# Performance work log

Measured on AMD Instinct MI355X. Metric: run time of the kernel, lower is better.

## Reference

```python
import jax, jax.numpy as jnp
import numpy as np

B, C, H, W = 8, 10, 128, 128  # batch, hidden_dim, spatial
EPS = 1e-5


def conv1x1(x, w, b=None):
    # x: [b, i, h, w], w: [o, i] -> [b, o, h, w]
    y = jnp.einsum('oi,bihw->bohw', w, x)
    if b is not None:
        y = y + b[None, :, None, None]
    return y


def bn(x, gamma, beta):
    # training-mode batchnorm over (N, H, W), as InPlaceABNSync(activation='none')
    m = x.mean(axis=(0, 2, 3), keepdims=True)
    v = x.var(axis=(0, 2, 3), keepdims=True)
    xn = (x - m) * jax.lax.rsqrt(v + EPS)
    return xn * gamma[None, :, None, None] + beta[None, :, None, None]


def conv_gru(x, h, wg, bg, wc):
    # ConvGRU with 1x1 kernels: gates conv -> 2 channels (reset, update)
    gates = conv1x1(jnp.concatenate([x, h], axis=1), wg, bg)  # [b,2,h,w]
    reset = jax.nn.sigmoid(gates[:, 0:1])
    update = jax.nn.sigmoid(gates[:, 1:2])
    cand = jnp.tanh(conv1x1(jnp.concatenate([x, reset * h], axis=1), wc))
    return (1.0 - update) * h + update * cand


def setup_inputs() -> dict:
    key = jax.random.key(0)
    ks = jax.random.split(key, 16)
    rn = lambda k, shape, s=1.0: jax.random.normal(k, shape, dtype=jnp.float32) * s
    inp = {
        'f0': rn(ks[0], (B, C, H, W)),
        'f1': rn(ks[1], (B, C, H, W)),
        'h0': rn(ks[2], (B, C, H, W)),
        'h1': rn(ks[3], (B, C, H, W)),
        'h2': rn(ks[4], (B, C, H, W)),
        # Composition.comp_att: Conv2d(2C -> 1, bias=True) + Sigmoid
        'W_att': rn(ks[5], (1, 2 * C), 0.1),
        'b_att': jnp.zeros((1,), jnp.float32),
        # Composition.relation: Conv(2C->2C, no bias) BN ReLU Conv(2C->C, no bias) BN ReLU
        'W_r1': rn(ks[6], (2 * C, 2 * C), 0.1),
        'g_r1': jnp.ones((2 * C,), jnp.float32),
        'be_r1': jnp.zeros((2 * C,), jnp.float32),
        'W_r2': rn(ks[7], (C, 2 * C), 0.1),
        'g_r2': jnp.ones((C,), jnp.float32),
        'be_r2': jnp.zeros((C,), jnp.float32),
        # ConvGRU update[0]: gates Conv(2C->2, bias) ; candidate Conv(2C->C, no bias)
        'Wg0': rn(ks[8], (2, 2 * C), 0.1),
        'bg0': jnp.zeros((2,), jnp.float32),
        'Wc0': rn(ks[9], (C, 2 * C), 0.1),
        # ConvGRU update[1]
        'Wg1': rn(ks[10], (2, 2 * C), 0.1),
        'bg1': jnp.zeros((2,), jnp.float32),
        'Wc1': rn(ks[11], (C, 2 * C), 0.1),
    }
    return inp


def reference(f0, f1, h0, h1, h2,
              W_att, b_att, W_r1, g_r1, be_r1, W_r2, g_r2, be_r2,
              Wg0, bg0, Wc0, Wg1, bg1, Wc1):
    # node 0: update[0](h_node_list[0], f_node_list[0])
    node0 = conv_gru(h0, f0, Wg0, bg0, Wc0)
    # Composition over children h1, h2
    comp_att = jax.nn.sigmoid(conv1x1(jnp.concatenate([h1, h2], axis=1), W_att, b_att))  # [b,1,h,w]
    x = jnp.concatenate([f1, (h1 + h2) * comp_att], axis=1)  # [b,2C,h,w]
    x = jax.nn.relu(bn(conv1x1(x, W_r1), g_r1, be_r1))
    comp_full = jax.nn.relu(bn(conv1x1(x, W_r2), g_r2, be_r2))  # [b,C,h,w]
    # node 1: update[1](comp_full, f_node_list[1])
    node1 = conv_gru(comp_full, f1, Wg1, bg1, Wc1)
    return node0, node1, comp_att
```

## Files before the change

kernel.cpp:

```cpp
#include <hip/hip_runtime.h>
#include <math.h>

#define HW     16384
#define CDIM   10
#define NPIX   131072
#define NPLANE 1310720
#define BN_N   131072.0f
#define EPS_BN 1e-5f

__device__ __forceinline__ float sigf(float x) { return 1.0f / (1.0f + __expf(-x)); }
__device__ __forceinline__ float tanh_fast(float x) {
    x = fminf(fmaxf(x, -15.0f), 15.0f);
    float e = __expf(2.0f * x);
    return (e - 1.0f) / (e + 1.0f);
}
__device__ __forceinline__ float wred(float v) {
#pragma unroll
    for (int o = 32; o; o >>= 1) v += __shfl_down(v, o, 64);
    return v;
}

__global__ __launch_bounds__(256) void kernA(
    const float* __restrict__ f0, const float* __restrict__ f1,
    const float* __restrict__ h0, const float* __restrict__ h1, const float* __restrict__ h2,
    const float* __restrict__ W_att, const float* __restrict__ b_att,
    const float* __restrict__ W_r1,
    const float* __restrict__ Wg0, const float* __restrict__ bg0, const float* __restrict__ Wc0,
    float* __restrict__ node0, float* __restrict__ att_out, float* __restrict__ stats1)
{
    __shared__ float sW1[400], sWatt[20], sWg[40], sWc[200];
    __shared__ float sPart[4 * 40];
    const int tid = threadIdx.x;
    for (int i = tid; i < 400; i += 256) sW1[i] = W_r1[i];
    for (int i = tid; i < 200; i += 256) sWc[i] = Wc0[i];
    if (tid < 20) sWatt[tid] = W_att[tid];
    if (tid < 40) sWg[tid] = Wg0[tid];
    __syncthreads();
    const float batt = b_att[0], bg_r = bg0[0], bg_u = bg0[1];
    const int p = blockIdx.x * 256 + tid;
    const int b = p >> 14, s = p & 16383;
    const int base = b * (CDIM * HW) + s;
    const int wave = tid >> 6, lane = tid & 63;

    float vh1[10], vh2[10], vf1[10];
#pragma unroll
    for (int c = 0; c < 10; c++) {
        vh1[c] = h1[base + c * HW];
        vh2[c] = h2[base + c * HW];
        vf1[c] = f1[base + c * HW];
    }
    float z = batt;
#pragma unroll
    for (int c = 0; c < 10; c++) z += sWatt[c] * vh1[c] + sWatt[10 + c] * vh2[c];
    const float att = sigf(z);
    att_out[p] = att;

    float x[20];
#pragma unroll
    for (int c = 0; c < 10; c++) { x[c] = vf1[c]; x[10 + c] = (vh1[c] + vh2[c]) * att; }
#pragma unroll
    for (int o = 0; o < 20; o++) {
        float acc = 0.0f;
#pragma unroll
        for (int i = 0; i < 20; i++) acc = fmaf(sW1[o * 20 + i], x[i], acc);
        float q = acc * acc;
        float rs = wred(acc);
        float rq = wred(q);
        if (lane == 0) { sPart[wave * 40 + o] = rs; sPart[wave * 40 + 20 + o] = rq; }
    }
    __syncthreads();
    if (tid < 40) {
        float t = sPart[tid] + sPart[40 + tid] + sPart[80 + tid] + sPart[120 + tid];
        atomicAdd(&stats1[tid], t);
    }

    float vf0[10], vh0[10];
#pragma unroll
    for (int c = 0; c < 10; c++) { vf0[c] = f0[base + c * HW]; vh0[c] = h0[base + c * HW]; }
    float g0 = bg_r, g1 = bg_u;
#pragma unroll
    for (int i = 0; i < 10; i++) {
        g0 += sWg[i] * vh0[i] + sWg[10 + i] * vf0[i];
        g1 += sWg[20 + i] * vh0[i] + sWg[30 + i] * vf0[i];
    }
    const float r = sigf(g0), u = sigf(g1);
#pragma unroll
    for (int o = 0; o < 10; o++) {
        float acc = 0.0f;
#pragma unroll
        for (int i = 0; i < 10; i++) acc = fmaf(sWc[o * 20 + i], vh0[i], acc);
#pragma unroll
        for (int i = 0; i < 10; i++) acc = fmaf(sWc[o * 20 + 10 + i], r * vf0[i], acc);
        node0[base + o * HW] = (1.0f - u) * vf0[o] + u * tanh_fast(acc);
    }
}

__global__ __launch_bounds__(256) void kernC(
    const float* __restrict__ f1, const float* __restrict__ h1, const float* __restrict__ h2,
    const float* __restrict__ att_in,
    const float* __restrict__ W_r1, const float* __restrict__ g_r1, const float* __restrict__ be_r1,
    const float* __restrict__ W_r2,
    const float* __restrict__ stats1, float* __restrict__ y2out, float* __restrict__ stats2)
{
    __shared__ float sW1[400], sW2[200], sA[20], sB[20];
    __shared__ float sPart[4 * 20];
    const int tid = threadIdx.x;
    for (int i = tid; i < 400; i += 256) sW1[i] = W_r1[i];
    for (int i = tid; i < 200; i += 256) sW2[i] = W_r2[i];
    if (tid < 20) {
        float sm = stats1[tid], sq = stats1[20 + tid];
        float mean = sm * (1.0f / BN_N);
        float var = sq * (1.0f / BN_N) - mean * mean;
        float a = g_r1[tid] * rsqrtf(var + EPS_BN);
        sA[tid] = a;
        sB[tid] = be_r1[tid] - mean * a;
    }
    __syncthreads();
    const int p = blockIdx.x * 256 + tid;
    const int b = p >> 14, s = p & 16383;
    const int base = b * (CDIM * HW) + s;
    const int wave = tid >> 6, lane = tid & 63;

    float vh1[10], vh2[10], vf1[10];
#pragma unroll
    for (int c = 0; c < 10; c++) {
        vh1[c] = h1[base + c * HW];
        vh2[c] = h2[base + c * HW];
        vf1[c] = f1[base + c * HW];
    }
    const float att = att_in[p];
    float x[20];
#pragma unroll
    for (int c = 0; c < 10; c++) { x[c] = vf1[c]; x[10 + c] = (vh1[c] + vh2[c]) * att; }
    float x2[20];
#pragma unroll
    for (int o = 0; o < 20; o++) {
        float acc = 0.0f;
#pragma unroll
        for (int i = 0; i < 20; i++) acc = fmaf(sW1[o * 20 + i], x[i], acc);
        x2[o] = fmaxf(fmaf(sA[o], acc, sB[o]), 0.0f);
    }
    const int base2 = b * (10 * HW) + s;
#pragma unroll
    for (int o = 0; o < 10; o++) {
        float acc = 0.0f;
#pragma unroll
        for (int i = 0; i < 20; i++) acc = fmaf(sW2[o * 20 + i], x2[i], acc);
        y2out[base2 + o * HW] = acc;
        float q = acc * acc;
        float rs = wred(acc);
        float rq = wred(q);
        if (lane == 0) { sPart[wave * 20 + o] = rs; sPart[wave * 20 + 10 + o] = rq; }
    }
    __syncthreads();
    if (tid < 20) {
        float t = sPart[tid] + sPart[20 + tid] + sPart[40 + tid] + sPart[60 + tid];
        atomicAdd(&stats2[tid], t);
    }
}

__global__ __launch_bounds__(256) void kernE(
    const float* __restrict__ f1, const float* __restrict__ y2in,
    const float* __restrict__ stats2,
    const float* __restrict__ g_r2, const float* __restrict__ be_r2,
    const float* __restrict__ Wg1, const float* __restrict__ bg1, const float* __restrict__ Wc1,
    float* __restrict__ node1)
{
    __shared__ float sWg[40], sWc[200], sA[10], sB[10];
    const int tid = threadIdx.x;
    for (int i = tid; i < 200; i += 256) sWc[i] = Wc1[i];
    if (tid < 40) sWg[tid] = Wg1[tid];
    if (tid < 10) {
        float sm = stats2[tid], sq = stats2[10 + tid];
        float mean = sm * (1.0f / BN_N);
        float var = sq * (1.0f / BN_N) - mean * mean;
        float a = g_r2[tid] * rsqrtf(var + EPS_BN);
        sA[tid] = a;
        sB[tid] = be_r2[tid] - mean * a;
    }
    __syncthreads();
    const float bg_r = bg1[0], bg_u = bg1[1];
    const int p = blockIdx.x * 256 + tid;
    const int b = p >> 14, s = p & 16383;
    const int base = b * (CDIM * HW) + s;

    float comp[10], vf1[10];
#pragma unroll
    for (int c = 0; c < 10; c++) {
        vf1[c] = f1[base + c * HW];
        comp[c] = fmaxf(fmaf(sA[c], y2in[base + c * HW], sB[c]), 0.0f);
    }
    float g0 = bg_r, g1 = bg_u;
#pragma unroll
    for (int i = 0; i < 10; i++) {
        g0 += sWg[i] * comp[i] + sWg[10 + i] * vf1[i];
        g1 += sWg[20 + i] * comp[i] + sWg[30 + i] * vf1[i];
    }
    const float r = sigf(g0), u = sigf(g1);
#pragma unroll
    for (int o = 0; o < 10; o++) {
        float acc = 0.0f;
#pragma unroll
        for (int i = 0; i < 10; i++) acc = fmaf(sWc[o * 20 + i], comp[i], acc);
#pragma unroll
        for (int i = 0; i < 10; i++) acc = fmaf(sWc[o * 20 + 10 + i], r * vf1[i], acc);
        node1[base + o * HW] = (1.0f - u) * vf1[o] + u * tanh_fast(acc);
    }
}

extern "C" void kernel_launch(void* const* d_in, const int* in_sizes, int n_in,
                              void* d_out, int out_size, void* d_ws, size_t ws_size,
                              hipStream_t stream) {
    const float* f0    = (const float*)d_in[0];
    const float* f1    = (const float*)d_in[1];
    const float* h0    = (const float*)d_in[2];
    const float* h1    = (const float*)d_in[3];
    const float* h2    = (const float*)d_in[4];
    const float* W_att = (const float*)d_in[5];
    const float* b_att = (const float*)d_in[6];
    const float* W_r1  = (const float*)d_in[7];
    const float* g_r1  = (const float*)d_in[8];
    const float* be_r1 = (const float*)d_in[9];
    const float* W_r2  = (const float*)d_in[10];
    const float* g_r2  = (const float*)d_in[11];
    const float* be_r2 = (const float*)d_in[12];
    const float* Wg0   = (const float*)d_in[13];
    const float* bg0   = (const float*)d_in[14];
    const float* Wc0   = (const float*)d_in[15];
    const float* Wg1   = (const float*)d_in[16];
    const float* bg1   = (const float*)d_in[17];
    const float* Wc1   = (const float*)d_in[18];

    float* out   = (float*)d_out;
    float* node0 = out;
    float* node1 = out + NPLANE;
    float* attO  = out + 2 * NPLANE;

    float* y2     = (float*)d_ws;
    float* stats1 = y2 + (size_t)10 * NPIX;
    float* stats2 = stats1 + 40;

    hipMemsetAsync(stats1, 0, 64 * sizeof(float), stream);

    dim3 grid(NPIX / 256), blk(256);
    kernA<<<grid, blk, 0, stream>>>(f0, f1, h0, h1, h2, W_att, b_att, W_r1,
                                    Wg0, bg0, Wc0, node0, attO, stats1);
    kernC<<<grid, blk, 0, stream>>>(f1, h1, h2, attO, W_r1, g_r1, be_r1, W_r2,
                                    stats1, y2, stats2);
    kernE<<<grid, blk, 0, stream>>>(f1, y2, stats2, g_r2, be_r2, Wg1, bg1, Wc1,
                                    node1);
}
```

Baseline: 148.2 us.

## Fuse three kernels into one cooperative kernel with grid syncs for batchnorm stats

Replaces the three-kernel pipeline with a single cooperative kernel that computes each pixel's activations once and holds them in registers. Grid-wide syncs wait for each batchnorm's statistics to finish accumulating before the next stage uses them. This removes the re-reads of h1/h2/f1/att, the y2 workspace round trip and two kernel launches, roughly halving memory traffic. In exchange it relies on all 512 blocks being co-resident, pays the cost of two grid barriers, and caps occupancy at two blocks per CU, which could cause register pressure or spills.

```diff
diff --git a/kernel.cpp b/kernel.cpp
--- a/kernel.cpp
+++ b/kernel.cpp
@@ -1,5 +1,8 @@
 #include <hip/hip_runtime.h>
+#include <hip/hip_cooperative_groups.h>
 #include <math.h>
+
+namespace cg = cooperative_groups;
 
 #define HW     16384
 #define CDIM   10
@@ -19,234 +22,206 @@
     for (int o = 32; o; o >>= 1) v += __shfl_down(v, o, 64);
     return v;
 }
-
-__global__ __launch_bounds__(256) void kernA(
-    const float* __restrict__ f0, const float* __restrict__ f1,
-    const float* __restrict__ h0, const float* __restrict__ h1, const float* __restrict__ h2,
-    const float* __restrict__ W_att, const float* __restrict__ b_att,
-    const float* __restrict__ W_r1,
-    const float* __restrict__ Wg0, const float* __restrict__ bg0, const float* __restrict__ Wc0,
-    float* __restrict__ node0, float* __restrict__ att_out, float* __restrict__ stats1)
+__device__ __forceinline__ float agent_load(const float* a) {
+    return __hip_atomic_load(a, __ATOMIC_RELAXED, __HIP_MEMORY_SCOPE_AGENT);
+}
+
+struct P {
+    const float *f0, *f1, *h0, *h1, *h2;
+    const float *W_att, *b_att;
+    const float *W_r1, *g_r1, *be_r1, *W_r2, *g_r2, *be_r2;
+    const float *Wg0, *bg0, *Wc0, *Wg1, *bg1, *Wc1;
+    float *node0, *node1, *attO;
+    float *stats;
+};
+
+__global__ __launch_bounds__(256, 2) void fused(P p)
 {
-    __shared__ float sW1[400], sWatt[20], sWg[40], sWc[200];
-    __shared__ float sPart[4 * 40];
-    const int tid = threadIdx.x;
-    for (int i = tid; i < 400; i += 256) sW1[i] = W_r1[i];
-    for (int i = tid; i < 200; i += 256) sWc[i] = Wc0[i];
-    if (tid < 20) sWatt[tid] = W_att[tid];
-    if (tid < 40) sWg[tid] = Wg0[tid];
-    __syncthreads();
-    const float batt = b_att[0], bg_r = bg0[0], bg_u = bg0[1];
-    const int p = blockIdx.x * 256 + tid;
-    const int b = p >> 14, s = p & 16383;
+    cg::grid_group grid = cg::this_grid();
+    __shared__ float sW1[400], sW2[200], sWc0[200], sWc1[200];
+    __shared__ float sWatt[20], sWg0[40], sWg1[40];
+    __shared__ float sAB[80];
+    __shared__ float sPart[160];
+    const int tid  = threadIdx.x;
+    const int wave = tid >> 6, lane = tid & 63;
+
+    for (int i = tid; i < 400; i += 256) sW1[i] = p.W_r1[i];
+    for (int i = tid; i < 200; i += 256) {
+        sW2[i]  = p.W_r2[i];
+        sWc0[i] = p.Wc0[i];
+        sWc1[i] = p.Wc1[i];
+    }
+    if (tid < 20) sWatt[tid] = p.W_att[tid];
+    if (tid < 40) { sWg0[tid] = p.Wg0[tid]; sWg1[tid] = p.Wg1[tid]; }
+    __syncthreads();
+
+    const int px   = blockIdx.x * 256 + tid;
+    const int b    = px >> 14, s = px & 16383;
     const int base = b * (CDIM * HW) + s;
-    const int wave = tid >> 6, lane = tid & 63;
-
-    float vh1[10], vh2[10], vf1[10];
-#pragma unroll
-    for (int c = 0; c < 10; c++) {
-        vh1[c] = h1[base + c * HW];
-        vh2[c] = h2[base + c * HW];
-        vf1[c] = f1[base + c * HW];
-    }
-    float z = batt;
-#pragma unroll
-    for (int c = 0; c < 10; c++) z += sWatt[c] * vh1[c] + sWatt[10 + c] * vh2[c];
-    const float att = sigf(z);
-    att_out[p] = att;
 
     float x[20];
-#pragma unroll
-    for (int c = 0; c < 10; c++) { x[c] = vf1[c]; x[10 + c] = (vh1[c] + vh2[c]) * att; }
-#pragma unroll
-    for (int o = 0; o < 20; o++) {
-        float acc = 0.0f;
-#pragma unroll
-        for (int i = 0; i < 20; i++) acc = fmaf(sW1[o * 20 + i], x[i], acc);
-        float q = acc * acc;
-        float rs = wred(acc);
-        float rq = wred(q);
-        if (lane == 0) { sPart[wave * 40 + o] = rs; sPart[wave * 40 + 20 + o] = rq; }
+    {
+        float vh1[10], vh2[10];
+#pragma unroll
+        for (int c = 0; c < 10; c++) {
+            vh1[c]  = p.h1[base + c * HW];
+            vh2[c]  = p.h2[base + c * HW];
+            x[c]    = p.f1[base + c * HW];
+        }
+        float z = p.b_att[0];
+#pragma unroll
+        for (int c = 0; c < 10; c++) z += sWatt[c] * vh1[c] + sWatt[10 + c] * vh2[c];
+        const float att = sigf(z);
+        p.attO[px] = att;
+#pragma unroll
+        for (int c = 0; c < 10; c++) x[10 + c] = (vh1[c] + vh2[c]) * att;
+
+#pragma unroll
+        for (int o = 0; o < 20; o++) {
+            float acc = 0.0f;
+#pragma unroll
+            for (int i = 0; i < 20; i++) acc = fmaf(sW1[o * 20 + i], x[i], acc);
+            float rs = wred(acc);
+            float rq = wred(acc * acc);
+            if (lane == 0) { sPart[wave * 40 + o] = rs; sPart[wave * 40 + 20 + o] = rq; }
+        }
+
+        float vf0[10], vh0[10];
+#pragma unroll
+        for (int c = 0; c < 10; c++) { vf0[c] = p.f0[base + c * HW]; vh0[c] = p.h0[base + c * HW]; }
+        float g0 = p.bg0[0], g1 = p.bg0[1];
+#pragma unroll
+        for (int i = 0; i < 10; i++) {
+            g0 += sWg0[i] * vh0[i] + sWg0[10 + i] * vf0[i];
+            g1 += sWg0[20 + i] * vh0[i] + sWg0[30 + i] * vf0[i];
+        }
+        const float r = sigf(g0), u = sigf(g1);
+#pragma unroll
+        for (int o = 0; o < 10; o++) {
+            float acc = 0.0f;
+#pragma unroll
+            for (int i = 0; i < 10; i++) acc = fmaf(sWc0[o * 20 + i], vh0[i], acc);
+#pragma unroll
+            for (int i = 0; i < 10; i++) acc = fmaf(sWc0[o * 20 + 10 + i], r * vf0[i], acc);
+            p.node0[base + o * HW] = (1.0f - u) * vf0[o] + u * tanh_fast(acc);
+        }
     }
     __syncthreads();
     if (tid < 40) {
         float t = sPart[tid] + sPart[40 + tid] + sPart[80 + tid] + sPart[120 + tid];
-        atomicAdd(&stats1[tid], t);
-    }
-
-    float vf0[10], vh0[10];
-#pragma unroll
-    for (int c = 0; c < 10; c++) { vf0[c] = f0[base + c * HW]; vh0[c] = h0[base + c * HW]; }
-    float g0 = bg_r, g1 = bg_u;
-#pragma unroll
-    for (int i = 0; i < 10; i++) {
-        g0 += sWg[i] * vh0[i] + sWg[10 + i] * vf0[i];
-        g1 += sWg[20 + i] * vh0[i] + sWg[30 + i] * vf0[i];
-    }
-    const float r = sigf(g0), u = sigf(g1);
-#pragma unroll
-    for (int o = 0; o < 10; o++) {
-        float acc = 0.0f;
-#pragma unroll
-        for (int i = 0; i < 10; i++) acc = fmaf(sWc[o * 20 + i], vh0[i], acc);
-#pragma unroll
-        for (int i = 0; i < 10; i++) acc = fmaf(sWc[o * 20 + 10 + i], r * vf0[i], acc);
-        node0[base + o * HW] = (1.0f - u) * vf0[o] + u * tanh_fast(acc);
-    }
-}
-
-__global__ __launch_bounds__(256) void kernC(
-    const float* __restrict__ f1, const float* __restrict__ h1, const float* __restrict__ h2,
-    const float* __restrict__ att_in,
-    const float* __restrict__ W_r1, const float* __restrict__ g_r1, const float* __restrict__ be_r1,
-    const float* __restrict__ W_r2,
-    const float* __restrict__ stats1, float* __restrict__ y2out, float* __restrict__ stats2)
-{
-    __shared__ float sW1[400], sW2[200], sA[20], sB[20];
-    __shared__ float sPart[4 * 20];
-    const int tid = threadIdx.x;
-    for (int i = tid; i < 400; i += 256) sW1[i] = W_r1[i];
-    for (int i = tid; i < 200; i += 256) sW2[i] = W_r2[i];
+        atomicAdd(&p.stats[tid], t);
+    }
+    __threadfence();
+    grid.sync();
+
     if (tid < 20) {
-        float sm = stats1[tid], sq = stats1[20 + tid];
+        float sm = agent_load(&p.stats[tid]);
+        float sq = agent_load(&p.stats[20 + tid]);
         float mean = sm * (1.0f / BN_N);
-        float var = sq * (1.0f / BN_N) - mean * mean;
-        float a = g_r1[tid] * rsqrtf(var + EPS_BN);
-        sA[tid] = a;
-        sB[tid] = be_r1[tid] - mean * a;
-    }
-    __syncthreads();
-    const int p = blockIdx.x * 256 + tid;
-    const int b = p >> 14, s = p & 16383;
-    const int base = b * (CDIM * HW) + s;
-    const int wave = tid >> 6, lane = tid & 63;
-
-    float vh1[10], vh2[10], vf1[10];
-#pragma unroll
-    for (int c = 0; c < 10; c++) {
-        vh1[c] = h1[base + c * HW];
-        vh2[c] = h2[base + c * HW];
-        vf1[c] = f1[base + c * HW];
-    }
-    const float att = att_in[p];
-    float x[20];
-#pragma unroll
-    for (int c = 0; c < 10; c++) { x[c] = vf1[c]; x[10 + c] = (vh1[c] + vh2[c]) * att; }
-    float x2[20];
-#pragma unroll
-    for (int o = 0; o < 20; o++) {
-        float acc = 0.0f;
-#pragma unroll
-        for (int i = 0; i < 20; i++) acc = fmaf(sW1[o * 20 + i], x[i], acc);
-        x2[o] = fmaxf(fmaf(sA[o], acc, sB[o]), 0.0f);
-    }
-    const int base2 = b * (10 * HW) + s;
-#pragma unroll
-    for (int o = 0; o < 10; o++) {
-        float acc = 0.0f;
-#pragma unroll
-        for (int i = 0; i < 20; i++) acc = fmaf(sW2[o * 20 + i], x2[i], acc);
-        y2out[base2 + o * HW] = acc;
-        float q = acc * acc;
-        float rs = wred(acc);
-        float rq = wred(q);
-        if (lane == 0) { sPart[wave * 20 + o] = rs; sPart[wave * 20 + 10 + o] = rq; }
+        float var  = sq * (1.0f / BN_N) - mean * mean;
+        float a = p.g_r1[tid] * rsqrtf(var + EPS_BN);
+        sAB[tid]      = a;
+        sAB[20 + tid] = p.be_r1[tid] - mean * a;
+    }
+    __syncthreads();
+
+    float y2[10];
+    {
+        float x2[20];
+#pragma unroll
+        for (int o = 0; o < 20; o++) {
+            float acc = 0.0f;
+#pragma unroll
+            for (int i = 0; i < 20; i++) acc = fmaf(sW1[o * 20 + i], x[i], acc);
+            x2[o] = fmaxf(fmaf(sAB[o], acc, sAB[20 + o]), 0.0f);
+        }
+#pragma unroll
+        for (int o = 0; o < 10; o++) {
+            float acc = 0.0f;
+#pragma unroll
+            for (int i = 0; i < 20; i++) acc = fmaf(sW2[o * 20 + i], x2[i], acc);
+            y2[o] = acc;
+            float rs = wred(acc);
+            float rq = wred(acc * acc);
+            if (lane == 0) { sPart[wave * 20 + o] = rs; sPart[wave * 20 + 10 + o] = rq; }
+        }
     }
     __syncthreads();
     if (tid < 20) {
         float t = sPart[tid] + sPart[20 + tid] + sPart[40 + tid] + sPart[60 + tid];
-        atomicAdd(&stats2[tid], t);
-    }
-}
-
-__global__ __launch_bounds__(256) void kernE(
-    const float* __restrict__ f1, const float* __restrict__ y2in,
-    const float* __restrict__ stats2,
-    const float* __restrict__ g_r2, const float* __restrict__ be_r2,
-    const float* __restrict__ Wg1, const float* __restrict__ bg1, const float* __restrict__ Wc1,
-    float* __restrict__ node1)
-{
-    __shared__ float sWg[40], sWc[200], sA[10], sB[10];
-    const int tid = threadIdx.x;
-    for (int i = tid; i < 200; i += 256) sWc[i] = Wc1[i];
-    if (tid < 40) sWg[tid] = Wg1[tid];
+        atomicAdd(&p.stats[40 + tid], t);
+    }
+    __threadfence();
+    grid.sync();
+
     if (tid < 10) {
-        float sm = stats2[tid], sq = stats2[10 + tid];
+        float sm = agent_load(&p.stats[40 + tid]);
+        float sq = agent_load(&p.stats[50 + tid]);
         float mean = sm * (1.0f / BN_N);
-        float var = sq * (1.0f / BN_N) - mean * mean;
-        float a = g_r2[tid] * rsqrtf(var + EPS_BN);
-        sA[tid] = a;
-        sB[tid] = be_r2[tid] - mean * a;
-    }
-    __syncthreads();
-    const float bg_r = bg1[0], bg_u = bg1[1];
-    const int p = blockIdx.x * 256 + tid;
-    const int b = p >> 14, s = p & 16383;
-    const int base = b * (CDIM * HW) + s;
-
-    float comp[10], vf1[10];
-#pragma unroll
-    for (int c = 0; c < 10; c++) {
-        vf1[c] = f1[base + c * HW];
-        comp[c] = fmaxf(fmaf(sA[c], y2in[base + c * HW], sB[c]), 0.0f);
-    }
-    float g0 = bg_r, g1 = bg_u;
-#pragma unroll
-    for (int i = 0; i < 10; i++) {
-        g0 += sWg[i] * comp[i] + sWg[10 + i] * vf1[i];
-        g1 += sWg[20 + i] * comp[i] + sWg[30 + i] * vf1[i];
-    }
-    const float r = sigf(g0), u = sigf(g1);
-#pragma unroll
-    for (int o = 0; o < 10; o++) {
-        float acc = 0.0f;
-#pragma unroll
-        for (int i = 0; i < 10; i++) acc = fmaf(sWc[o * 20 + i], comp[i], acc);
-#pragma unroll
-        for (int i = 0; i < 10; i++) acc = fmaf(sWc[o * 20 + 10 + i], r * vf1[i], acc);
-        node1[base + o * HW] = (1.0f - u) * vf1[o] + u * tanh_fast(acc);
+        float var  = sq * (1.0f / BN_N) - mean * mean;
+        float a = p.g_r2[tid] * rsqrtf(var + EPS_BN);
+        sAB[40 + tid] = a;
+        sAB[50 + tid] = p.be_r2[tid] - mean * a;
+    }
+    __syncthreads();
+
+    {
+        float comp[10];
+#pragma unroll
+        for (int c = 0; c < 10; c++)
+            comp[c] = fmaxf(fmaf(sAB[40 + c], y2[c], sAB[50 + c]), 0.0f);
+        float g0 = p.bg1[0], g1 = p.bg1[1];
+#pragma unroll
+        for (int i = 0; i < 10; i++) {
+            g0 += sWg1[i] * comp[i] + sWg1[10 + i] * x[i];
+            g1 += sWg1[20 + i] * comp[i] + sWg1[30 + i] * x[i];
+        }
+        const float r = sigf(g0), u = sigf(g1);
+#pragma unroll
+        for (int o = 0; o < 10; o++) {
+            float acc = 0.0f;
+#pragma unroll
+            for (int i = 0; i < 10; i++) acc = fmaf(sWc1[o * 20 + i], comp[i], acc);
+#pragma unroll
+            for (int i = 0; i < 10; i++) acc = fmaf(sWc1[o * 20 + 10 + i], r * x[i], acc);
+            p.node1[base + o * HW] = (1.0f - u) * x[o] + u * tanh_fast(acc);
+        }
     }
 }
 
 extern "C" void kernel_launch(void* const* d_in, const int* in_sizes, int n_in,
                               void* d_out, int out_size, void* d_ws, size_t ws_size,
                               hipStream_t stream) {
-    const float* f0    = (const float*)d_in[0];
-    const float* f1    = (const float*)d_in[1];
-    const float* h0    = (const float*)d_in[2];
-    const float* h1    = (const float*)d_in[3];
-    const float* h2    = (const float*)d_in[4];
-    const float* W_att = (const float*)d_in[5];
-    const float* b_att = (const float*)d_in[6];
-    const float* W_r1  = (const float*)d_in[7];
-    const float* g_r1  = (const float*)d_in[8];
-    const float* be_r1 = (const float*)d_in[9];
-    const float* W_r2  = (const float*)d_in[10];
-    const float* g_r2  = (const float*)d_in[11];
-    const float* be_r2 = (const float*)d_in[12];
-    const float* Wg0   = (const float*)d_in[13];
-    const float* bg0   = (const float*)d_in[14];
-    const float* Wc0   = (const float*)d_in[15];
-    const float* Wg1   = (const float*)d_in[16];
-    const float* bg1   = (const float*)d_in[17];
-    const float* Wc1   = (const float*)d_in[18];
-
-    float* out   = (float*)d_out;
-    float* node0 = out;
-    float* node1 = out + NPLANE;
-    float* attO  = out + 2 * NPLANE;
-
-    float* y2     = (float*)d_ws;
-    float* stats1 = y2 + (size_t)10 * NPIX;
-    float* stats2 = stats1 + 40;
-
-    hipMemsetAsync(stats1, 0, 64 * sizeof(float), stream);
-
-    dim3 grid(NPIX / 256), blk(256);
-    kernA<<<grid, blk, 0, stream>>>(f0, f1, h0, h1, h2, W_att, b_att, W_r1,
-                                    Wg0, bg0, Wc0, node0, attO, stats1);
-    kernC<<<grid, blk, 0, stream>>>(f1, h1, h2, attO, W_r1, g_r1, be_r1, W_r2,
-                                    stats1, y2, stats2);
-    kernE<<<grid, blk, 0, stream>>>(f1, y2, stats2, g_r2, be_r2, Wg1, bg1, Wc1,
-                                    node1);
-}
+    P p;
+    p.f0    = (const float*)d_in[0];
+    p.f1    = (const float*)d_in[1];
+    p.h0    = (const float*)d_in[2];
+    p.h1    = (const float*)d_in[3];
+    p.h2    = (const float*)d_in[4];
+    p.W_att = (const float*)d_in[5];
+    p.b_att = (const float*)d_in[6];
+    p.W_r1  = (const float*)d_in[7];
+    p.g_r1  = (const float*)d_in[8];
+    p.be_r1 = (const float*)d_in[9];
+    p.W_r2  = (const float*)d_in[10];
+    p.g_r2  = (const float*)d_in[11];
+    p.be_r2 = (const float*)d_in[12];
+    p.Wg0   = (const float*)d_in[13];
+    p.bg0   = (const float*)d_in[14];
+    p.Wc0   = (const float*)d_in[15];
+    p.Wg1   = (const float*)d_in[16];
+    p.bg1   = (const float*)d_in[17];
+    p.Wc1   = (const float*)d_in[18];
+
+    float* out = (float*)d_out;
+    p.node0 = out;
+    p.node1 = out + NPLANE;
+    p.attO  = out + 2 * NPLANE;
+    p.stats = (float*)d_ws;
+
+    hipMemsetAsync(p.stats, 0, 64 * sizeof(float), stream);
+
+    void* args[] = { &p };
+    hipLaunchCooperativeKernel((void*)fused, dim3(NPIX / 256), dim3(256),
+                               args, 0, stream);
+}
```

New measurement: 350.0 us. 136% more time.

## Replace atomic BN stats with per-block partials; hoist loads; nontemporal output stores

Applied to the files above, without the earlier changes.

Each block now writes its batchnorm sum and sum-of-squares partials to a per-block workspace slot instead of doing atomicAdd. Every block of the next kernel reduces all 512 partials itself, which removes the memset launch and the atomic contention. All global input loads are moved ahead of the shared-weight fill and the stats reduction so memory latency overlaps that setup work. Outputs node0 and node1 use nontemporal stores. The cost is a redundant 512x64 partial read in every block of kernC and kernE, and higher register pressure from keeping all 50 inputs live in kernA.

```diff
diff --git a/kernel.cpp b/kernel.cpp
--- a/kernel.cpp
+++ b/kernel.cpp
@@ -5,6 +5,7 @@
 #define CDIM   10
 #define NPIX   131072
 #define NPLANE 1310720
+#define NBLK   512
 #define BN_N   131072.0f
 #define EPS_BN 1e-5f
 
@@ -26,34 +27,36 @@
     const float* __restrict__ W_att, const float* __restrict__ b_att,
     const float* __restrict__ W_r1,
     const float* __restrict__ Wg0, const float* __restrict__ bg0, const float* __restrict__ Wc0,
-    float* __restrict__ node0, float* __restrict__ att_out, float* __restrict__ stats1)
+    float* __restrict__ node0, float* __restrict__ att_out, float* __restrict__ part1)
 {
     __shared__ float sW1[400], sWatt[20], sWg[40], sWc[200];
     __shared__ float sPart[4 * 40];
     const int tid = threadIdx.x;
+    const int wave = tid >> 6, lane = tid & 63;
+    const int px = blockIdx.x * 256 + tid;
+    const int b = px >> 14, s = px & 16383;
+    const int base = b * (CDIM * HW) + s;
+
+    float vh1[10], vh2[10], vf1[10], vf0[10], vh0[10];
+#pragma unroll
+    for (int c = 0; c < 10; c++) {
+        vh1[c] = h1[base + c * HW];
+        vh2[c] = h2[base + c * HW];
+        vf1[c] = f1[base + c * HW];
+        vf0[c] = f0[base + c * HW];
+        vh0[c] = h0[base + c * HW];
+    }
     for (int i = tid; i < 400; i += 256) sW1[i] = W_r1[i];
     for (int i = tid; i < 200; i += 256) sWc[i] = Wc0[i];
     if (tid < 20) sWatt[tid] = W_att[tid];
     if (tid < 40) sWg[tid] = Wg0[tid];
     __syncthreads();
-    const float batt = b_att[0], bg_r = bg0[0], bg_u = bg0[1];
-    const int p = blockIdx.x * 256 + tid;
-    const int b = p >> 14, s = p & 16383;
-    const int base = b * (CDIM * HW) + s;
-    const int wave = tid >> 6, lane = tid & 63;
-
-    float vh1[10], vh2[10], vf1[10];
-#pragma unroll
-    for (int c = 0; c < 10; c++) {
-        vh1[c] = h1[base + c * HW];
-        vh2[c] = h2[base + c * HW];
-        vf1[c] = f1[base + c * HW];
-    }
-    float z = batt;
+
+    float z = b_att[0];
 #pragma unroll
     for (int c = 0; c < 10; c++) z += sWatt[c] * vh1[c] + sWatt[10 + c] * vh2[c];
     const float att = sigf(z);
-    att_out[p] = att;
+    att_out[px] = att;
 
     float x[20];
 #pragma unroll
@@ -63,21 +66,12 @@
         float acc = 0.0f;
 #pragma unroll
         for (int i = 0; i < 20; i++) acc = fmaf(sW1[o * 20 + i], x[i], acc);
-        float q = acc * acc;
         float rs = wred(acc);
-        float rq = wred(q);
+        float rq = wred(acc * acc);
         if (lane == 0) { sPart[wave * 40 + o] = rs; sPart[wave * 40 + 20 + o] = rq; }
     }
-    __syncthreads();
-    if (tid < 40) {
-        float t = sPart[tid] + sPart[40 + tid] + sPart[80 + tid] + sPart[120 + tid];
-        atomicAdd(&stats1[tid], t);
-    }
-
-    float vf0[10], vh0[10];
-#pragma unroll
-    for (int c = 0; c < 10; c++) { vf0[c] = f0[base + c * HW]; vh0[c] = h0[base + c * HW]; }
-    float g0 = bg_r, g1 = bg_u;
+
+    float g0 = bg0[0], g1 = bg0[1];
 #pragma unroll
     for (int i = 0; i < 10; i++) {
         g0 += sWg[i] * vh0[i] + sWg[10 + i] * vf0[i];
@@ -91,7 +85,16 @@
         for (int i = 0; i < 10; i++) acc = fmaf(sWc[o * 20 + i], vh0[i], acc);
 #pragma unroll
         for (int i = 0; i < 10; i++) acc = fmaf(sWc[o * 20 + 10 + i], r * vf0[i], acc);
-        node0[base + o * HW] = (1.0f - u) * vf0[o] + u * tanh_fast(acc);
+        __builtin_nontemporal_store((1.0f - u) * vf0[o] + u * tanh_fast(acc),
+                                    &node0[base + o * HW]);
+    }
+
+    __syncthreads();
+    if (tid < 64) {
+        float t = 0.0f;
+        if (tid < 40)
+            t = sPart[tid] + sPart[40 + tid] + sPart[80 + tid] + sPart[120 + tid];
+        part1[blockIdx.x * 64 + tid] = t;
     }
 }
 
@@ -100,26 +103,16 @@
     const float* __restrict__ att_in,
     const float* __restrict__ W_r1, const float* __restrict__ g_r1, const float* __restrict__ be_r1,
     const float* __restrict__ W_r2,
-    const float* __restrict__ stats1, float* __restrict__ y2out, float* __restrict__ stats2)
+    const float* __restrict__ part1, float* __restrict__ y2out, float* __restrict__ part2)
 {
-    __shared__ float sW1[400], sW2[200], sA[20], sB[20];
+    __shared__ float sW1[400], sW2[200], sAB[40];
+    __shared__ float sRed[256];
     __shared__ float sPart[4 * 20];
     const int tid = threadIdx.x;
-    for (int i = tid; i < 400; i += 256) sW1[i] = W_r1[i];
-    for (int i = tid; i < 200; i += 256) sW2[i] = W_r2[i];
-    if (tid < 20) {
-        float sm = stats1[tid], sq = stats1[20 + tid];
-        float mean = sm * (1.0f / BN_N);
-        float var = sq * (1.0f / BN_N) - mean * mean;
-        float a = g_r1[tid] * rsqrtf(var + EPS_BN);
-        sA[tid] = a;
-        sB[tid] = be_r1[tid] - mean * a;
-    }
-    __syncthreads();
-    const int p = blockIdx.x * 256 + tid;
-    const int b = p >> 14, s = p & 16383;
+    const int wave = tid >> 6, lane = tid & 63;
+    const int px = blockIdx.x * 256 + tid;
+    const int b = px >> 14, s = px & 16383;
     const int base = b * (CDIM * HW) + s;
-    const int wave = tid >> 6, lane = tid & 63;
 
     float vh1[10], vh2[10], vf1[10];
 #pragma unroll
@@ -128,7 +121,30 @@
         vh2[c] = h2[base + c * HW];
         vf1[c] = f1[base + c * HW];
     }
-    const float att = att_in[p];
+    const float att = att_in[px];
+
+    for (int i = tid; i < 400; i += 256) sW1[i] = W_r1[i];
+    for (int i = tid; i < 200; i += 256) sW2[i] = W_r2[i];
+
+    {
+        const int j = tid & 63, q = tid >> 6;
+        float acc = 0.0f;
+#pragma unroll 8
+        for (int bb = q; bb < NBLK; bb += 4) acc += part1[bb * 64 + j];
+        sRed[tid] = acc;
+    }
+    __syncthreads();
+    if (tid < 20) {
+        float sm = sRed[tid]       + sRed[64 + tid]      + sRed[128 + tid]      + sRed[192 + tid];
+        float sq = sRed[20 + tid]  + sRed[84 + tid]      + sRed[148 + tid]      + sRed[212 + tid];
+        float mean = sm * (1.0f / BN_N);
+        float var  = sq * (1.0f / BN_N) - mean * mean;
+        float a = g_r1[tid] * rsqrtf(var + EPS_BN);
+        sAB[tid]      = a;
+        sAB[20 + tid] = be_r1[tid] - mean * a;
+    }
+    __syncthreads();
+
     float x[20];
 #pragma unroll
     for (int c = 0; c < 10; c++) { x[c] = vf1[c]; x[10 + c] = (vh1[c] + vh2[c]) * att; }
@@ -138,7 +154,7 @@
         float acc = 0.0f;
 #pragma unroll
         for (int i = 0; i < 20; i++) acc = fmaf(sW1[o * 20 + i], x[i], acc);
-        x2[o] = fmaxf(fmaf(sA[o], acc, sB[o]), 0.0f);
+        x2[o] = fmaxf(fmaf(sAB[o], acc, sAB[20 + o]), 0.0f);
     }
     const int base2 = b * (10 * HW) + s;
 #pragma unroll
@@ -147,50 +163,66 @@
 #pragma unroll
         for (int i = 0; i < 20; i++) acc = fmaf(sW2[o * 20 + i], x2[i], acc);
         y2out[base2 + o * HW] = acc;
-        float q = acc * acc;
         float rs = wred(acc);
-        float rq = wred(q);
+        float rq = wred(acc * acc);
         if (lane == 0) { sPart[wave * 20 + o] = rs; sPart[wave * 20 + 10 + o] = rq; }
     }
     __syncthreads();
-    if (tid < 20) {
-        float t = sPart[tid] + sPart[20 + tid] + sPart[40 + tid] + sPart[60 + tid];
-        atomicAdd(&stats2[tid], t);
+    if (tid < 64) {
+        float t = 0.0f;
+        if (tid < 20)
+            t = sPart[tid] + sPart[20 + tid] + sPart[40 + tid] + sPart[60 + tid];
+        part2[blockIdx.x * 64 + tid] = t;
     }
 }
 
 __global__ __launch_bounds__(256) void kernE(
     const float* __restrict__ f1, const float* __restrict__ y2in,
-    const float* __restrict__ stats2,
+    const float* __restrict__ part2,
     const float* __restrict__ g_r2, const float* __restrict__ be_r2,
     const float* __restrict__ Wg1, const float* __restrict__ bg1, const float* __restrict__ Wc1,
     float* __restrict__ node1)
 {
-    __shared__ float sWg[40], sWc[200], sA[10], sB[10];
+    __shared__ float sWg[40], sWc[200], sAB[20];
+    __shared__ float sRed[256];
     const int tid = threadIdx.x;
+    const int px = blockIdx.x * 256 + tid;
+    const int b = px >> 14, s = px & 16383;
+    const int base = b * (CDIM * HW) + s;
+
+    float vf1[10], vy2[10];
+#pragma unroll
+    for (int c = 0; c < 10; c++) {
+        vf1[c] = f1[base + c * HW];
+        vy2[c] = y2in[base + c * HW];
+    }
     for (int i = tid; i < 200; i += 256) sWc[i] = Wc1[i];
     if (tid < 40) sWg[tid] = Wg1[tid];
+
+    {
+        const int j = tid & 63, q = tid >> 6;
+        float acc = 0.0f;
+#pragma unroll 8
+        for (int bb = q; bb < NBLK; bb += 4) acc += part2[bb * 64 + j];
+        sRed[tid] = acc;
+    }
+    __syncthreads();
     if (tid < 10) {
-        float sm = stats2[tid], sq = stats2[10 + tid];
+        float sm = sRed[tid]      + sRed[64 + tid]      + sRed[128 + tid]      + sRed[192 + tid];
+        float sq = sRed[10 + tid] + sRed[74 + tid]      + sRed[138 + tid]      + sRed[202 + tid];
         float mean = sm * (1.0f / BN_N);
-        float var = sq * (1.0f / BN_N) - mean * mean;
+        float var  = sq * (1.0f / BN_N) - mean * mean;
         float a = g_r2[tid] * rsqrtf(var + EPS_BN);
-        sA[tid] = a;
-        sB[tid] = be_r2[tid] - mean * a;
-    }
-    __syncthreads();
-    const float bg_r = bg1[0], bg_u = bg1[1];
-    const int p = blockIdx.x * 256 + tid;
-    const int b = p >> 14, s = p & 16383;
-    const int base = b * (CDIM * HW) + s;
-
-    float comp[10], vf1[10];
-#pragma unroll
-    for (int c = 0; c < 10; c++) {
-        vf1[c] = f1[base + c * HW];
-        comp[c] = fmaxf(fmaf(sA[c], y2in[base + c * HW], sB[c]), 0.0f);
-    }
-    float g0 = bg_r, g1 = bg_u;
+        sAB[tid]      = a;
+        sAB[10 + tid] = be_r2[tid] - mean * a;
+    }
+    __syncthreads();
+
+    float comp[10];
+#pragma unroll
+    for (int c = 0; c < 10; c++)
+        comp[c] = fmaxf(fmaf(sAB[c], vy2[c], sAB[10 + c]), 0.0f);
+    float g0 = bg1[0], g1 = bg1[1];
 #pragma unroll
     for (int i = 0; i < 10; i++) {
         g0 += sWg[i] * comp[i] + sWg[10 + i] * vf1[i];
@@ -204,7 +236,8 @@
         for (int i = 0; i < 10; i++) acc = fmaf(sWc[o * 20 + i], comp[i], acc);
 #pragma unroll
         for (int i = 0; i < 10; i++) acc = fmaf(sWc[o * 20 + 10 + i], r * vf1[i], acc);
-        node1[base + o * HW] = (1.0f - u) * vf1[o] + u * tanh_fast(acc);
+        __builtin_nontemporal_store((1.0f - u) * vf1[o] + u * tanh_fast(acc),
+                                    &node1[base + o * HW]);
     }
 }
 
@@ -236,17 +269,15 @@
     float* node1 = out + NPLANE;
     float* attO  = out + 2 * NPLANE;
 
-    float* y2     = (float*)d_ws;
-    float* stats1 = y2 + (size_t)10 * NPIX;
-    float* stats2 = stats1 + 40;
-
-    hipMemsetAsync(stats1, 0, 64 * sizeof(float), stream);
-
-    dim3 grid(NPIX / 256), blk(256);
+    float* y2    = (float*)d_ws;
+    float* part1 = y2 + (size_t)10 * NPIX;
+    float* part2 = part1 + (size_t)NBLK * 64;
+
+    dim3 grid(NBLK), blk(256);
     kernA<<<grid, blk, 0, stream>>>(f0, f1, h0, h1, h2, W_att, b_att, W_r1,
-                                    Wg0, bg0, Wc0, node0, attO, stats1);
+                                    Wg0, bg0, Wc0, node0, attO, part1);
     kernC<<<grid, blk, 0, stream>>>(f1, h1, h2, attO, W_r1, g_r1, be_r1, W_r2,
-                                    stats1, y2, stats2);
-    kernE<<<grid, blk, 0, stream>>>(f1, y2, stats2, g_r2, be_r2, Wg1, bg1, Wc1,
+                                    part1, y2, part2);
+    kernE<<<grid, blk, 0, stream>>>(f1, y2, part2, g_r2, be_r2, Wg1, bg1, Wc1,
                                     node1);
 }
```

Result: slower. 168.4 us (+13.6%).

## Process two pixels per thread with float2 loads and nontemporal stores

Applied to the files above, without the earlier changes.

Each thread now handles two adjacent pixels using 8-byte vector loads, and writes outputs with nontemporal stores. Blocks shrink to 128 threads. Weights are read straight from global/scalar memory instead of being staged in shared memory. kernC recomputes the attention instead of re-reading it, and BN coefficients are computed per thread rather than once per block. The aim is fewer memory instructions and less sync overhead, at the cost of more registers and some redundant arithmetic.

```diff
diff --git a/kernel.cpp b/kernel.cpp
--- a/kernel.cpp
+++ b/kernel.cpp
@@ -2,11 +2,15 @@
 #include <math.h>
 
 #define HW     16384
-#define CDIM   10
 #define NPIX   131072
 #define NPLANE 1310720
+#define NG     65536
+#define TPB    128
+#define NBLK   (NG / TPB)
 #define BN_N   131072.0f
 #define EPS_BN 1e-5f
+
+typedef float v2f __attribute__((ext_vector_type(2)));
 
 __device__ __forceinline__ float sigf(float x) { return 1.0f / (1.0f + __expf(-x)); }
 __device__ __forceinline__ float tanh_fast(float x) {
@@ -19,192 +23,221 @@
     for (int o = 32; o; o >>= 1) v += __shfl_down(v, o, 64);
     return v;
 }
-
-__global__ __launch_bounds__(256) void kernA(
+__device__ __forceinline__ float2 ld2(const float* p) {
+    return *(const float2*)p;
+}
+__device__ __forceinline__ void nt_store2(float2 v, float* p) {
+    v2f t; t.x = v.x; t.y = v.y;
+    __builtin_nontemporal_store(t, (v2f*)p);
+}
+
+__global__ __launch_bounds__(TPB, 1) void kernA(
     const float* __restrict__ f0, const float* __restrict__ f1,
     const float* __restrict__ h0, const float* __restrict__ h1, const float* __restrict__ h2,
     const float* __restrict__ W_att, const float* __restrict__ b_att,
     const float* __restrict__ W_r1,
     const float* __restrict__ Wg0, const float* __restrict__ bg0, const float* __restrict__ Wc0,
-    float* __restrict__ node0, float* __restrict__ att_out, float* __restrict__ stats1)
+    float* __restrict__ node0, float* __restrict__ att_out, float* __restrict__ stats)
 {
-    __shared__ float sW1[400], sWatt[20], sWg[40], sWc[200];
-    __shared__ float sPart[4 * 40];
-    const int tid = threadIdx.x;
-    for (int i = tid; i < 400; i += 256) sW1[i] = W_r1[i];
-    for (int i = tid; i < 200; i += 256) sWc[i] = Wc0[i];
-    if (tid < 20) sWatt[tid] = W_att[tid];
-    if (tid < 40) sWg[tid] = Wg0[tid];
+    __shared__ float sPart[2 * 40];
+    const int tid = threadIdx.x, wave = tid >> 6, lane = tid & 63;
+    const int g = blockIdx.x * TPB + tid;
+    const int b = g >> 13, sp = (g & 8191) << 1;
+    const int base = b * (10 * HW) + sp;
+
+    float2 vf0[10], vf1[10], vh0[10], vh1[10], vh2[10];
+#pragma unroll
+    for (int c = 0; c < 10; c++) {
+        vh1[c] = ld2(h1 + base + c * HW);
+        vh2[c] = ld2(h2 + base + c * HW);
+        vf1[c] = ld2(f1 + base + c * HW);
+        vf0[c] = ld2(f0 + base + c * HW);
+        vh0[c] = ld2(h0 + base + c * HW);
+    }
+
+    float zx = b_att[0], zy = zx;
+#pragma unroll
+    for (int c = 0; c < 10; c++) {
+        zx += W_att[c] * vh1[c].x + W_att[10 + c] * vh2[c].x;
+        zy += W_att[c] * vh1[c].y + W_att[10 + c] * vh2[c].y;
+    }
+    const float ax_ = sigf(zx), ay_ = sigf(zy);
+    nt_store2(make_float2(ax_, ay_), att_out + 2 * g);
+
+    float2 x[20];
+#pragma unroll
+    for (int c = 0; c < 10; c++) {
+        x[c] = vf1[c];
+        x[10 + c] = make_float2((vh1[c].x + vh2[c].x) * ax_,
+                                (vh1[c].y + vh2[c].y) * ay_);
+    }
+#pragma unroll
+    for (int o = 0; o < 20; o++) {
+        float sx = 0.0f, sy = 0.0f;
+#pragma unroll
+        for (int i = 0; i < 20; i++) {
+            const float w = W_r1[o * 20 + i];
+            sx = fmaf(w, x[i].x, sx);
+            sy = fmaf(w, x[i].y, sy);
+        }
+        float rs = wred(sx + sy);
+        float rq = wred(sx * sx + sy * sy);
+        if (lane == 0) { sPart[wave * 40 + o] = rs; sPart[wave * 40 + 20 + o] = rq; }
+    }
+
+    float g0x = bg0[0], g1x = bg0[1], g0y = bg0[0], g1y = bg0[1];
+#pragma unroll
+    for (int i = 0; i < 10; i++) {
+        g0x += Wg0[i] * vh0[i].x + Wg0[10 + i] * vf0[i].x;
+        g0y += Wg0[i] * vh0[i].y + Wg0[10 + i] * vf0[i].y;
+        g1x += Wg0[20 + i] * vh0[i].x + Wg0[30 + i] * vf0[i].x;
+        g1y += Wg0[20 + i] * vh0[i].y + Wg0[30 + i] * vf0[i].y;
+    }
+    const float rx = sigf(g0x), ux = sigf(g1x);
+    const float ry = sigf(g0y), uy = sigf(g1y);
+#pragma unroll
+    for (int o = 0; o < 10; o++) {
+        float cx = 0.0f, cy = 0.0f;
+#pragma unroll
+        for (int i = 0; i < 10; i++) {
+            const float w0 = Wc0[o * 20 + i], w1 = Wc0[o * 20 + 10 + i];
+            cx = fmaf(w0, vh0[i].x, cx); cx = fmaf(w1, rx * vf0[i].x, cx);
+            cy = fmaf(w0, vh0[i].y, cy); cy = fmaf(w1, ry * vf0[i].y, cy);
+        }
+        nt_store2(make_float2((1.0f - ux) * vf0[o].x + ux * tanh_fast(cx),
+                              (1.0f - uy) * vf0[o].y + uy * tanh_fast(cy)),
+                  node0 + base + o * HW);
+    }
+
     __syncthreads();
-    const float batt = b_att[0], bg_r = bg0[0], bg_u = bg0[1];
-    const int p = blockIdx.x * 256 + tid;
-    const int b = p >> 14, s = p & 16383;
-    const int base = b * (CDIM * HW) + s;
-    const int wave = tid >> 6, lane = tid & 63;
-
-    float vh1[10], vh2[10], vf1[10];
-#pragma unroll
-    for (int c = 0; c < 10; c++) {
-        vh1[c] = h1[base + c * HW];
-        vh2[c] = h2[base + c * HW];
-        vf1[c] = f1[base + c * HW];
-    }
-    float z = batt;
-#pragma unroll
-    for (int c = 0; c < 10; c++) z += sWatt[c] * vh1[c] + sWatt[10 + c] * vh2[c];
-    const float att = sigf(z);
-    att_out[p] = att;
-
-    float x[20];
-#pragma unroll
-    for (int c = 0; c < 10; c++) { x[c] = vf1[c]; x[10 + c] = (vh1[c] + vh2[c]) * att; }
-#pragma unroll
-    for (int o = 0; o < 20; o++) {
-        float acc = 0.0f;
-#pragma unroll
-        for (int i = 0; i < 20; i++) acc = fmaf(sW1[o * 20 + i], x[i], acc);
-        float q = acc * acc;
-        float rs = wred(acc);
-        float rq = wred(q);
-        if (lane == 0) { sPart[wave * 40 + o] = rs; sPart[wave * 40 + 20 + o] = rq; }
-    }
-    __syncthreads();
-    if (tid < 40) {
-        float t = sPart[tid] + sPart[40 + tid] + sPart[80 + tid] + sPart[120 + tid];
-        atomicAdd(&stats1[tid], t);
-    }
-
-    float vf0[10], vh0[10];
-#pragma unroll
-    for (int c = 0; c < 10; c++) { vf0[c] = f0[base + c * HW]; vh0[c] = h0[base + c * HW]; }
-    float g0 = bg_r, g1 = bg_u;
-#pragma unroll
-    for (int i = 0; i < 10; i++) {
-        g0 += sWg[i] * vh0[i] + sWg[10 + i] * vf0[i];
-        g1 += sWg[20 + i] * vh0[i] + sWg[30 + i] * vf0[i];
-    }
-    const float r = sigf(g0), u = sigf(g1);
-#pragma unroll
-    for (int o = 0; o < 10; o++) {
-        float acc = 0.0f;
-#pragma unroll
-        for (int i = 0; i < 10; i++) acc = fmaf(sWc[o * 20 + i], vh0[i], acc);
-#pragma unroll
-        for (int i = 0; i < 10; i++) acc = fmaf(sWc[o * 20 + 10 + i], r * vf0[i], acc);
-        node0[base + o * HW] = (1.0f - u) * vf0[o] + u * tanh_fast(acc);
-    }
-}
-
-__global__ __launch_bounds__(256) void kernC(
+    if (tid < 40) atomicAdd(&stats[tid], sPart[tid] + sPart[40 + tid]);
+}
+
+__global__ __launch_bounds__(TPB, 1) void kernC(
     const float* __restrict__ f1, const float* __restrict__ h1, const float* __restrict__ h2,
-    const float* __restrict__ att_in,
+    const float* __restrict__ W_att, const float* __restrict__ b_att,
     const float* __restrict__ W_r1, const float* __restrict__ g_r1, const float* __restrict__ be_r1,
     const float* __restrict__ W_r2,
-    const float* __restrict__ stats1, float* __restrict__ y2out, float* __restrict__ stats2)
+    float* __restrict__ stats, float* __restrict__ y2out)
 {
-    __shared__ float sW1[400], sW2[200], sA[20], sB[20];
-    __shared__ float sPart[4 * 20];
-    const int tid = threadIdx.x;
-    for (int i = tid; i < 400; i += 256) sW1[i] = W_r1[i];
-    for (int i = tid; i < 200; i += 256) sW2[i] = W_r2[i];
-    if (tid < 20) {
-        float sm = stats1[tid], sq = stats1[20 + tid];
-        float mean = sm * (1.0f / BN_N);
-        float var = sq * (1.0f / BN_N) - mean * mean;
-        float a = g_r1[tid] * rsqrtf(var + EPS_BN);
-        sA[tid] = a;
-        sB[tid] = be_r1[tid] - mean * a;
+    __shared__ float sPart[2 * 20];
+    const int tid = threadIdx.x, wave = tid >> 6, lane = tid & 63;
+    const int g = blockIdx.x * TPB + tid;
+    const int b = g >> 13, sp = (g & 8191) << 1;
+    const int base = b * (10 * HW) + sp;
+
+    float2 vf1[10], vh1[10], vh2[10];
+#pragma unroll
+    for (int c = 0; c < 10; c++) {
+        vh1[c] = ld2(h1 + base + c * HW);
+        vh2[c] = ld2(h2 + base + c * HW);
+        vf1[c] = ld2(f1 + base + c * HW);
+    }
+
+    float zx = b_att[0], zy = zx;
+#pragma unroll
+    for (int c = 0; c < 10; c++) {
+        zx += W_att[c] * vh1[c].x + W_att[10 + c] * vh2[c].x;
+        zy += W_att[c] * vh1[c].y + W_att[10 + c] * vh2[c].y;
+    }
+    const float ax_ = sigf(zx), ay_ = sigf(zy);
+
+    float2 x[20];
+#pragma unroll
+    for (int c = 0; c < 10; c++) {
+        x[c] = vf1[c];
+        x[10 + c] = make_float2((vh1[c].x + vh2[c].x) * ax_,
+                                (vh1[c].y + vh2[c].y) * ay_);
+    }
+
+    float2 x2[20];
+#pragma unroll
+    for (int o = 0; o < 20; o++) {
+        float sx = 0.0f, sy = 0.0f;
+#pragma unroll
+        for (int i = 0; i < 20; i++) {
+            const float w = W_r1[o * 20 + i];
+            sx = fmaf(w, x[i].x, sx);
+            sy = fmaf(w, x[i].y, sy);
+        }
+        const float mean = stats[o] * (1.0f / BN_N);
+        const float var  = stats[20 + o] * (1.0f / BN_N) - mean * mean;
+        const float a = g_r1[o] * rsqrtf(var + EPS_BN);
+        const float bb = be_r1[o] - mean * a;
+        x2[o] = make_float2(fmaxf(fmaf(a, sx, bb), 0.0f),
+                            fmaxf(fmaf(a, sy, bb), 0.0f));
+    }
+
+#pragma unroll
+    for (int o = 0; o < 10; o++) {
+        float sx = 0.0f, sy = 0.0f;
+#pragma unroll
+        for (int i = 0; i < 20; i++) {
+            const float w = W_r2[o * 20 + i];
+            sx = fmaf(w, x2[i].x, sx);
+            sy = fmaf(w, x2[i].y, sy);
+        }
+        *(float2*)(y2out + base + o * HW) = make_float2(sx, sy);
+        float rs = wred(sx + sy);
+        float rq = wred(sx * sx + sy * sy);
+        if (lane == 0) { sPart[wave * 20 + o] = rs; sPart[wave * 20 + 10 + o] = rq; }
     }
     __syncthreads();
-    const int p = blockIdx.x * 256 + tid;
-    const int b = p >> 14, s = p & 16383;
-    const int base = b * (CDIM * HW) + s;
-    const int wave = tid >> 6, lane = tid & 63;
-
-    float vh1[10], vh2[10], vf1[10];
-#pragma unroll
-    for (int c = 0; c < 10; c++) {
-        vh1[c] = h1[base + c * HW];
-        vh2[c] = h2[base + c * HW];
-        vf1[c] = f1[base + c * HW];
-    }
-    const float att = att_in[p];
-    float x[20];
-#pragma unroll
-    for (int c = 0; c < 10; c++) { x[c] = vf1[c]; x[10 + c] = (vh1[c] + vh2[c]) * att; }
-    float x2[20];
-#pragma unroll
-    for (int o = 0; o < 20; o++) {
-        float acc = 0.0f;
-#pragma unroll
-        for (int i = 0; i < 20; i++) acc = fmaf(sW1[o * 20 + i], x[i], acc);
-        x2[o] = fmaxf(fmaf(sA[o], acc, sB[o]), 0.0f);
-    }
-    const int base2 = b * (10 * HW) + s;
-#pragma unroll
-    for (int o = 0; o < 10; o++) {
-        float acc = 0.0f;
-#pragma unroll
-        for (int i = 0; i < 20; i++) acc = fmaf(sW2[o * 20 + i], x2[i], acc);
-        y2out[base2 + o * HW] = acc;
-        float q = acc * acc;
-        float rs = wred(acc);
-        float rq = wred(q);
-        if (lane == 0) { sPart[wave * 20 + o] = rs; sPart[wave * 20 + 10 + o] = rq; }
-    }
-    __syncthreads();
-    if (tid < 20) {
-        float t = sPart[tid] + sPart[20 + tid] + sPart[40 + tid] + sPart[60 + tid];
-        atomicAdd(&stats2[tid], t);
-    }
-}
-
-__global__ __launch_bounds__(256) void kernE(
+    if (tid < 20) atomicAdd(&stats[40 + tid], sPart[tid] + sPart[20 + tid]);
+}
+
+__global__ __launch_bounds__(TPB, 1) void kernE(
     const float* __restrict__ f1, const float* __restrict__ y2in,
-    const float* __restrict__ stats2,
+    const float* __restrict__ stats,
     const float* __restrict__ g_r2, const float* __restrict__ be_r2,
     const float* __restrict__ Wg1, const float* __restrict__ bg1, const float* __restrict__ Wc1,
     float* __restrict__ node1)
 {
-    __shared__ float sWg[40], sWc[200], sA[10], sB[10];
     const int tid = threadIdx.x;
-    for (int i = tid; i < 200; i += 256) sWc[i] = Wc1[i];
-    if (tid < 40) sWg[tid] = Wg1[tid];
-    if (tid < 10) {
-        float sm = stats2[tid], sq = stats2[10 + tid];
-        float mean = sm * (1.0f / BN_N);
-        float var = sq * (1.0f / BN_N) - mean * mean;
-        float a = g_r2[tid] * rsqrtf(var + EPS_BN);
-        sA[tid] = a;
-        sB[tid] = be_r2[tid] - mean * a;
-    }
-    __syncthreads();
-    const float bg_r = bg1[0], bg_u = bg1[1];
-    const int p = blockIdx.x * 256 + tid;
-    const int b = p >> 14, s = p & 16383;
-    const int base = b * (CDIM * HW) + s;
-
-    float comp[10], vf1[10];
-#pragma unroll
-    for (int c = 0; c < 10; c++) {
-        vf1[c] = f1[base + c * HW];
-        comp[c] = fmaxf(fmaf(sA[c], y2in[base + c * HW], sB[c]), 0.0f);
-    }
-    float g0 = bg_r, g1 = bg_u;
+    const int g = blockIdx.x * TPB + tid;
+    const int b = g >> 13, sp = (g & 8191) << 1;
+    const int base = b * (10 * HW) + sp;
+
+    float2 vf1[10], vy2[10];
+#pragma unroll
+    for (int c = 0; c < 10; c++) {
+        vf1[c] = ld2(f1 + base + c * HW);
+        vy2[c] = ld2(y2in + base + c * HW);
+    }
+
+    float2 comp[10];
+#pragma unroll
+    for (int c = 0; c < 10; c++) {
+        const float mean = stats[40 + c] * (1.0f / BN_N);
+        const float var  = stats[50 + c] * (1.0f / BN_N) - mean * mean;
+        const float a = g_r2[c] * rsqrtf(var + EPS_BN);
+        const float bb = be_r2[c] - mean * a;
+        comp[c] = make_float2(fmaxf(fmaf(a, vy2[c].x, bb), 0.0f),
+                              fmaxf(fmaf(a, vy2[c].y, bb), 0.0f));
+    }
+
+    float g0x = bg1[0], g1x = bg1[1], g0y = bg1[0], g1y = bg1[1];
 #pragma unroll
     for (int i = 0; i < 10; i++) {
-        g0 += sWg[i] * comp[i] + sWg[10 + i] * vf1[i];
-        g1 += sWg[20 + i] * comp[i] + sWg[30 + i] * vf1[i];
-    }
-    const float r = sigf(g0), u = sigf(g1);
+        g0x += Wg1[i] * comp[i].x + Wg1[10 + i] * vf1[i].x;
+        g0y += Wg1[i] * comp[i].y + Wg1[10 + i] * vf1[i].y;
+        g1x += Wg1[20 + i] * comp[i].x + Wg1[30 + i] * vf1[i].x;
+        g1y += Wg1[20 + i] * comp[i].y + Wg1[30 + i] * vf1[i].y;
+    }
+    const float rx = sigf(g0x), ux = sigf(g1x);
+    const float ry = sigf(g0y), uy = sigf(g1y);
 #pragma unroll
     for (int o = 0; o < 10; o++) {
-        float acc = 0.0f;
-#pragma unroll
-        for (int i = 0; i < 10; i++) acc = fmaf(sWc[o * 20 + i], comp[i], acc);
-#pragma unroll
-        for (int i = 0; i < 10; i++) acc = fmaf(sWc[o * 20 + 10 + i], r * vf1[i], acc);
-        node1[base + o * HW] = (1.0f - u) * vf1[o] + u * tanh_fast(acc);
+        float cx = 0.0f, cy = 0.0f;
+#pragma unroll
+        for (int i = 0; i < 10; i++) {
+            const float w0 = Wc1[o * 20 + i], w1 = Wc1[o * 20 + 10 + i];
+            cx = fmaf(w0, comp[i].x, cx); cx = fmaf(w1, rx * vf1[i].x, cx);
+            cy = fmaf(w0, comp[i].y, cy); cy = fmaf(w1, ry * vf1[i].y, cy);
+        }
+        nt_store2(make_float2((1.0f - ux) * vf1[o].x + ux * tanh_fast(cx),
+                              (1.0f - uy) * vf1[o].y + uy * tanh_fast(cy)),
+                  node1 + base + o * HW);
     }
 }
 
@@ -236,17 +269,16 @@
     float* node1 = out + NPLANE;
     float* attO  = out + 2 * NPLANE;
 
-    float* y2     = (float*)d_ws;
-    float* stats1 = y2 + (size_t)10 * NPIX;
-    float* stats2 = stats1 + 40;
-
-    hipMemsetAsync(stats1, 0, 64 * sizeof(float), stream);
-
-    dim3 grid(NPIX / 256), blk(256);
+    float* stats = (float*)d_ws;
+    float* y2    = stats + 64;
+
+    hipMemsetAsync(stats, 0, 64 * sizeof(float), stream);
+
+    dim3 grid(NBLK), blk(TPB);
     kernA<<<grid, blk, 0, stream>>>(f0, f1, h0, h1, h2, W_att, b_att, W_r1,
-                                    Wg0, bg0, Wc0, node0, attO, stats1);
-    kernC<<<grid, blk, 0, stream>>>(f1, h1, h2, attO, W_r1, g_r1, be_r1, W_r2,
-                                    stats1, y2, stats2);
-    kernE<<<grid, blk, 0, stream>>>(f1, y2, stats2, g_r2, be_r2, Wg1, bg1, Wc1,
+                                    Wg0, bg0, Wc0, node0, attO, stats);
+    kernC<<<grid, blk, 0, stream>>>(f1, h1, h2, W_att, b_att, W_r1, g_r1, be_r1,
+                                    W_r2, stats, y2);
+    kernE<<<grid, blk, 0, stream>>>(f1, y2, stats, g_r2, be_r2, Wg1, bg1, Wc1,
                                     node1);
 }
```

Measured after the change: 158.5 us. 7.0% more time.
